# Kernel tuning notes

Hardware: AMD Instinct MI355X
Metric: run time of the kernel (lower is better)

The kernel has to match this reference:

```python
import jax, jax.numpy as jnp
import numpy as np

N_NODES = 50000
N_EDGES = 800000
IN_CH = 128
HID_CH = 128
OUT_CH = 10
NUM_GRAPHS = 128


def setup_inputs() -> dict:
    key = jax.random.key(0)
    ks = jax.random.split(key, 10)
    x = jax.random.normal(ks[0], (N_NODES, IN_CH), dtype=jnp.float32)
    edge_index = jax.random.randint(ks[1], (2, N_EDGES), 0, N_NODES, dtype=jnp.int64)
    batch = jnp.sort(jax.random.randint(ks[2], (N_NODES,), 0, NUM_GRAPHS, dtype=jnp.int64))
    s1 = 1.0 / np.sqrt(IN_CH)
    s2 = 1.0 / np.sqrt(HID_CH)
    W1 = jax.random.uniform(ks[3], (IN_CH, HID_CH), jnp.float32, -s1, s1)
    b1 = jnp.zeros((HID_CH,), jnp.float32)
    W2 = jax.random.uniform(ks[4], (HID_CH, HID_CH), jnp.float32, -s2, s2)
    b2 = jnp.zeros((HID_CH,), jnp.float32)
    Wc = jax.random.uniform(ks[5], (HID_CH, OUT_CH), jnp.float32, -s2, s2)
    bc = jax.random.uniform(ks[6], (OUT_CH,), jnp.float32, -s2, s2)
    return {"x": x, "edge_index": edge_index, "batch": batch,
            "W1": W1, "b1": b1, "W2": W2, "b2": b2, "Wc": Wc, "bc": bc}


def _gcn_norm(edge_index, num_nodes):
    # add self-loops, compute symmetric normalization deg^-1/2[src]*deg^-1/2[dst]
    loop = jnp.arange(num_nodes, dtype=edge_index.dtype)
    src = jnp.concatenate([edge_index[0], loop])
    dst = jnp.concatenate([edge_index[1], loop])
    deg = jax.ops.segment_sum(jnp.ones_like(dst, dtype=jnp.float32), dst,
                              num_segments=num_nodes)
    dinv = jnp.where(deg > 0, jax.lax.rsqrt(deg), 0.0)
    norm = dinv[src] * dinv[dst]
    return src, dst, norm


def _gcn_conv(h, src, dst, norm, W, b, num_nodes):
    h = h @ W                                    # [N, out]
    msg = h[src] * norm[:, None]                 # [E+N, out] gather + scale
    agg = jax.ops.segment_sum(msg, dst, num_segments=num_nodes)
    return agg + b


def reference(x, edge_index, batch, W1, b1, W2, b2, Wc, bc):
    n = x.shape[0]
    src, dst, norm = _gcn_norm(edge_index, n)
    h = jax.nn.relu(_gcn_conv(x, src, dst, norm, W1, b1, n))
    h = jax.nn.relu(_gcn_conv(h, src, dst, norm, W2, b2, n))
    # global mean pool over graphs
    sums = jax.ops.segment_sum(h, batch, num_segments=NUM_GRAPHS)
    cnts = jax.ops.segment_sum(jnp.ones((n,), jnp.float32), batch,
                               num_segments=NUM_GRAPHS)
    pooled = sums / jnp.maximum(cnts, 1.0)[:, None]
    # dropout is identity in eval mode
    return pooled @ Wc + bc
```

## Files before the change

### kernel.cpp

```cpp
#include <hip/hip_runtime.h>

#define N_NODES 50000
#define N_EDGES 800000
#define CH 128
#define NOUT 10
#define NUM_GRAPHS 128
#define POOL_CHUNK 50
#define GR 64
#define GEMM_BLOCKS ((N_NODES + GR - 1) / GR)
#define FILL_SEGS 128
#define FILL_CHUNK (N_EDGES / FILL_SEGS)
#define DST_RANGE (N_NODES / 8)
#define DEG_CAP 64

typedef __attribute__((ext_vector_type(8))) short bf16x8;
typedef __attribute__((ext_vector_type(4))) float f32x4;

union FragU { uint4 u; bf16x8 s; };

__device__ __forceinline__ unsigned pack_bf16(float a, float b) {
    unsigned ua = __float_as_uint(a), ub = __float_as_uint(b);
    ua += 0x7fffu + ((ua >> 16) & 1u);
    ub += 0x7fffu + ((ub >> 16) & 1u);
    return (ua >> 16) | (ub & 0xffff0000u);
}

__device__ __forceinline__ unsigned short cvt_bf16(float v) {
    unsigned u = __float_as_uint(v);
    u += 0x7fffu + ((u >> 16) & 1u);
    return (unsigned short)(u >> 16);
}

__global__ __launch_bounds__(256) void k_prep(const float* __restrict__ W1,
                                              const float* __restrict__ W2,
                                              unsigned short* __restrict__ Wb1,
                                              unsigned short* __restrict__ Wb2,
                                              int* __restrict__ fill_pos,
                                              float* __restrict__ psum) {
    if (blockIdx.x < 2) {
        const float* W = blockIdx.x ? W2 : W1;
        unsigned short* Wb = blockIdx.x ? Wb2 : Wb1;
        for (int i = threadIdx.x; i < CH * CH; i += 256) {
            int k = i >> 7, n = i & 127;
            Wb[((((k >> 3) << 7) + n) << 3) + (k & 7)] = cvt_bf16(W[i]);
        }
    } else if (blockIdx.x < 198) {
        int idx = (blockIdx.x - 2) * 256 + threadIdx.x;
        if (idx < N_NODES) fill_pos[idx] = 0;
    } else {
        psum[(blockIdx.x - 198) * 256 + threadIdx.x] = 0.f;
    }
}

template <bool SCALE>
__device__ __forceinline__ void gemm_body9(const float* __restrict__ X,
                                           const unsigned short* __restrict__ Wb,
                                           unsigned short* __restrict__ Yb,
                                           const int* __restrict__ cnt,
                                           int bid) {
    const int tid = threadIdx.x;
    const int w = tid >> 6;
    const int lane = tid & 63;
    const int m = lane & 15;
    const int quad = lane >> 4;
    const int row0 = bid * GR + w * 16;

    int row_a = row0 + m;
    if (row_a > N_NODES - 1) row_a = N_NODES - 1;
    const float4* Xr = (const float4*)(X + (size_t)row_a * CH) + quad * 2;

    f32x4 acc[8];
    #pragma unroll
    for (int ct = 0; ct < 8; ++ct) acc[ct] = (f32x4){0.f, 0.f, 0.f, 0.f};

    const uint4* Wq = (const uint4*)Wb;
    #pragma unroll
    for (int ks = 0; ks < 4; ++ks) {
        float4 a0 = Xr[ks * 8];
        float4 a1 = Xr[ks * 8 + 1];
        FragU af;
        af.u.x = pack_bf16(a0.x, a0.y);
        af.u.y = pack_bf16(a0.z, a0.w);
        af.u.z = pack_bf16(a1.x, a1.y);
        af.u.w = pack_bf16(a1.z, a1.w);
        const int kg = ks * 4 + quad;
        #pragma unroll
        for (int ct = 0; ct < 8; ++ct) {
            FragU bfu;
            bfu.u = Wq[kg * 128 + ct * 16 + m];
            acc[ct] = __builtin_amdgcn_mfma_f32_16x16x32_bf16(af.s, bfu.s, acc[ct], 0, 0, 0);
        }
    }

    #pragma unroll
    for (int r = 0; r < 4; ++r) {
        int row = row0 + quad * 4 + r;
        if (row < N_NODES) {
            float dv = SCALE ? rsqrtf((float)(cnt[row] + 1)) : 1.0f;
            unsigned short* yrow = Yb + (size_t)row * CH + m;
            #pragma unroll
            for (int ct = 0; ct < 8; ++ct)
                yrow[ct * 16] = cvt_bf16(SCALE ? acc[ct][r] * dv : acc[ct][r]);
        }
    }
}

__global__ __launch_bounds__(256) void k_gemm_fill(const float* __restrict__ X,
                                                   const unsigned short* __restrict__ Wb,
                                                   unsigned short* __restrict__ Yb,
                                                   const int* __restrict__ src,
                                                   const int* __restrict__ dst,
                                                   int* __restrict__ fill_pos,
                                                   int* __restrict__ csr_src) {
    if (blockIdx.x < GEMM_BLOCKS) {
        gemm_body9<false>(X, Wb, Yb, nullptr, blockIdx.x);
    } else {
        const int b = blockIdx.x - GEMM_BLOCKS;
        const int rng = b & 7;
        const int seg = b >> 3;
        const int lo = rng * DST_RANGE, hi = lo + DST_RANGE;
        const int base = seg * FILL_CHUNK;
        for (int it = 0; it < FILL_CHUNK; it += 256) {
            int e = base + it + threadIdx.x;
            if (it + (int)threadIdx.x < FILL_CHUNK) {
                int d = dst[e];
                if (d >= lo && d < hi) {
                    int slot = atomicAdd(&fill_pos[d], 1);
                    if (slot < DEG_CAP) csr_src[(d << 6) + slot] = src[e];
                }
            }
        }
    }
}

__global__ __launch_bounds__(256) void k_gemm9b(const float* __restrict__ X,
                                                const unsigned short* __restrict__ Wb,
                                                unsigned short* __restrict__ Yb,
                                                const int* __restrict__ cnt) {
    gemm_body9<true>(X, Wb, Yb, cnt, blockIdx.x);
}

__global__ __launch_bounds__(256) void k_gather1(const unsigned* __restrict__ tb,
                                                 const int* __restrict__ csr_src,
                                                 const int* __restrict__ cnt,
                                                 const float* __restrict__ b,
                                                 float* __restrict__ h) {
    const int wid = threadIdx.x >> 6;
    const int lane = threadIdx.x & 63;
    const int v = blockIdx.x * 4 + wid;

    int len = cnt[v];
    const float dv = rsqrtf((float)(len + 1));
    if (len > DEG_CAP) len = DEG_CAP;

    float x0 = 0.f, y0 = 0.f, x1 = 0.f, y1 = 0.f;
    float x2 = 0.f, y2 = 0.f, x3 = 0.f, y3 = 0.f;

    int u_l = 0;
    float w_l = 0.f;
    if (lane < len) {
        u_l = csr_src[(v << 6) + lane];
        w_l = rsqrtf((float)(cnt[u_l] + 1));
    }
    int j = 0;
    for (; j + 3 < len; j += 4) {
        int u0 = __shfl(u_l, j),     u1 = __shfl(u_l, j + 1);
        int u2 = __shfl(u_l, j + 2), u3 = __shfl(u_l, j + 3);
        float w0 = __shfl(w_l, j),     w1 = __shfl(w_l, j + 1);
        float w2 = __shfl(w_l, j + 2), w3 = __shfl(w_l, j + 3);
        unsigned r0 = tb[(size_t)u0 * 64 + lane];
        unsigned r1 = tb[(size_t)u1 * 64 + lane];
        unsigned r2 = tb[(size_t)u2 * 64 + lane];
        unsigned r3 = tb[(size_t)u3 * 64 + lane];
        x0 = fmaf(w0, __uint_as_float(r0 << 16), x0);
        y0 = fmaf(w0, __uint_as_float(r0 & 0xffff0000u), y0);
        x1 = fmaf(w1, __uint_as_float(r1 << 16), x1);
        y1 = fmaf(w1, __uint_as_float(r1 & 0xffff0000u), y1);
        x2 = fmaf(w2, __uint_as_float(r2 << 16), x2);
        y2 = fmaf(w2, __uint_as_float(r2 & 0xffff0000u), y2);
        x3 = fmaf(w3, __uint_as_float(r3 << 16), x3);
        y3 = fmaf(w3, __uint_as_float(r3 & 0xffff0000u), y3);
    }
    for (; j < len; ++j) {
        int u = __shfl(u_l, j);
        float w = __shfl(w_l, j);
        unsigned r = tb[(size_t)u * 64 + lane];
        x0 = fmaf(w, __uint_as_float(r << 16), x0);
        y0 = fmaf(w, __uint_as_float(r & 0xffff0000u), y0);
    }

    unsigned rs = tb[(size_t)v * 64 + lane];
    float sx = x0 + x1 + x2 + x3 + dv * __uint_as_float(rs << 16);
    float sy = y0 + y1 + y2 + y3 + dv * __uint_as_float(rs & 0xffff0000u);
    float2 bb = ((const float2*)b)[lane];
    float2 o;
    o.x = fmaxf(fmaf(dv, sx, bb.x), 0.f);
    o.y = fmaxf(fmaf(dv, sy, bb.y), 0.f);
    ((float2*)h)[(size_t)v * 64 + lane] = o;
}

__global__ __launch_bounds__(256) void k_gather2(const unsigned* __restrict__ tb,
                                                 const int* __restrict__ csr_src,
                                                 const int* __restrict__ cnt,
                                                 const float* __restrict__ b,
                                                 float* __restrict__ h) {
    const int wid = threadIdx.x >> 6;
    const int lane = threadIdx.x & 63;
    const int v = blockIdx.x * 4 + wid;

    int len = cnt[v];
    const float dv = rsqrtf((float)(len + 1));
    if (len > DEG_CAP) len = DEG_CAP;

    float x0 = 0.f, y0 = 0.f, x1 = 0.f, y1 = 0.f;
    float x2 = 0.f, y2 = 0.f, x3 = 0.f, y3 = 0.f;

    int u_l = 0;
    if (lane < len) u_l = csr_src[(v << 6) + lane];
    int j = 0;
    for (; j + 3 < len; j += 4) {
        int u0 = __shfl(u_l, j),     u1 = __shfl(u_l, j + 1);
        int u2 = __shfl(u_l, j + 2), u3 = __shfl(u_l, j + 3);
        unsigned r0 = tb[(size_t)u0 * 64 + lane];
        unsigned r1 = tb[(size_t)u1 * 64 + lane];
        unsigned r2 = tb[(size_t)u2 * 64 + lane];
        unsigned r3 = tb[(size_t)u3 * 64 + lane];
        x0 += __uint_as_float(r0 << 16); y0 += __uint_as_float(r0 & 0xffff0000u);
        x1 += __uint_as_float(r1 << 16); y1 += __uint_as_float(r1 & 0xffff0000u);
        x2 += __uint_as_float(r2 << 16); y2 += __uint_as_float(r2 & 0xffff0000u);
        x3 += __uint_as_float(r3 << 16); y3 += __uint_as_float(r3 & 0xffff0000u);
    }
    for (; j < len; ++j) {
        int u = __shfl(u_l, j);
        unsigned r = tb[(size_t)u * 64 + lane];
        x0 += __uint_as_float(r << 16); y0 += __uint_as_float(r & 0xffff0000u);
    }

    unsigned rs = tb[(size_t)v * 64 + lane];
    float sx = x0 + x1 + x2 + x3 + __uint_as_float(rs << 16);
    float sy = y0 + y1 + y2 + y3 + __uint_as_float(rs & 0xffff0000u);
    float2 bb = ((const float2*)b)[lane];
    float2 o;
    o.x = fmaxf(fmaf(dv, sx, bb.x), 0.f);
    o.y = fmaxf(fmaf(dv, sy, bb.y), 0.f);
    ((float2*)h)[(size_t)v * 64 + lane] = o;
}

__global__ __launch_bounds__(128) void k_pool2(const float* __restrict__ h,
                                               const int* __restrict__ batch,
                                               float* __restrict__ psum) {
    const int c = threadIdx.x;
    const int v0 = blockIdx.x * POOL_CHUNK;
    __shared__ int bg[POOL_CHUNK];
    if (c < POOL_CHUNK) bg[c] = batch[v0 + c];
    __syncthreads();

    float acc = 0.f;
    int g = bg[0];
    #pragma unroll 5
    for (int j = 0; j < POOL_CHUNK; ++j) {
        int bgj = bg[j];
        float val = h[(size_t)(v0 + j) * CH + c];
        if (bgj != g) {
            atomicAdd(&psum[g * CH + c], acc);
            acc = 0.f;
            g = bgj;
        }
        acc += val;
    }
    atomicAdd(&psum[g * CH + c], acc);
}

__global__ __launch_bounds__(128) void k_classify(const float* __restrict__ psum,
                                                  const int* __restrict__ batch,
                                                  const float* __restrict__ Wc,
                                                  const float* __restrict__ bc,
                                                  float* __restrict__ out) {
    __shared__ float p[CH];
    __shared__ float sinv;
    int g = blockIdx.x;
    int tid = threadIdx.x;
    if (tid == 0) {
        int lo = 0, hi = N_NODES;
        while (lo < hi) { int mid = (lo + hi) >> 1; if (batch[mid] < g) lo = mid + 1; else hi = mid; }
        int start = lo;
        lo = 0; hi = N_NODES;
        while (lo < hi) { int mid = (lo + hi) >> 1; if (batch[mid] < g + 1) lo = mid + 1; else hi = mid; }
        sinv = 1.0f / fmaxf((float)(lo - start), 1.0f);
    }
    __syncthreads();
    p[tid] = psum[g * CH + tid] * sinv;
    __syncthreads();
    if (tid < NOUT) {
        float acc = bc[tid];
        #pragma unroll 4
        for (int k = 0; k < CH; ++k) acc += p[k] * Wc[k * NOUT + tid];
        out[g * NOUT + tid] = acc;
    }
}

extern "C" void kernel_launch(void* const* d_in, const int* in_sizes, int n_in,
                              void* d_out, int out_size, void* d_ws, size_t ws_size,
                              hipStream_t stream) {
    const float* x     = (const float*)d_in[0];
    const int*   ei    = (const int*)d_in[1];
    const int*   batch = (const int*)d_in[2];
    const float* W1    = (const float*)d_in[3];
    const float* b1    = (const float*)d_in[4];
    const float* W2    = (const float*)d_in[5];
    const float* b2    = (const float*)d_in[6];
    const float* Wc    = (const float*)d_in[7];
    const float* bc    = (const float*)d_in[8];
    float* out = (float*)d_out;

    const int* src = ei;
    const int* dst = ei + N_EDGES;

    int*            fill_pos = (int*)d_ws;
    int*            csr_src  = fill_pos + N_NODES;
    unsigned short* wb1      = (unsigned short*)(csr_src + (size_t)N_NODES * DEG_CAP);
    unsigned short* wb2      = wb1 + CH * CH;
    unsigned short* tb       = wb2 + CH * CH;
    float*          hbuf     = (float*)(tb + (size_t)N_NODES * CH);
    float*          psum     = hbuf + (size_t)N_NODES * CH;

    k_prep<<<198 + 64, 256, 0, stream>>>(W1, W2, wb1, wb2, fill_pos, psum);

    k_gemm_fill<<<GEMM_BLOCKS + FILL_SEGS * 8, 256, 0, stream>>>(
        x, wb1, tb, src, dst, fill_pos, csr_src);

    k_gather1<<<N_NODES / 4, 256, 0, stream>>>((unsigned*)tb, csr_src, fill_pos, b1, hbuf);

    k_gemm9b<<<GEMM_BLOCKS, 256, 0, stream>>>(hbuf, wb2, tb, fill_pos);

    k_gather2<<<N_NODES / 4, 256, 0, stream>>>((unsigned*)tb, csr_src, fill_pos, b2, hbuf);

    k_pool2<<<N_NODES / POOL_CHUNK, 128, 0, stream>>>(hbuf, batch, psum);
    k_classify<<<NUM_GRAPHS, 128, 0, stream>>>(psum, batch, Wc, bc, out);
}
```

Baseline: 260.1 us.

## Fuse mean-pool into second gather, widen gather loads, vectorize CSR fill

The second GCN aggregation now accumulates pooled graph sums directly through shared memory and atomics, so the separate pool kernel and the store and reload of the layer-2 hidden buffer are gone. Both gather kernels switch to 16-byte loads, with each wave processing four neighbours at once in 16-lane subgroups and combining them with cross-lane shuffle reductions. The CSR fill reads dst as int4 and uses more segments, and the GEMM issues all of its X loads before the MFMA loop. In exchange it adds a block-level sync and shuffle-reduction overhead, and the fill assumes the chunk size is divisible by four.

```diff
diff --git a/kernel.cpp b/kernel.cpp
--- a/kernel.cpp
+++ b/kernel.cpp
@@ -5,10 +5,9 @@
 #define CH 128
 #define NOUT 10
 #define NUM_GRAPHS 128
-#define POOL_CHUNK 50
 #define GR 64
 #define GEMM_BLOCKS ((N_NODES + GR - 1) / GR)
-#define FILL_SEGS 128
+#define FILL_SEGS 200
 #define FILL_CHUNK (N_EDGES / FILL_SEGS)
 #define DST_RANGE (N_NODES / 8)
 #define DEG_CAP 64
@@ -69,6 +68,13 @@
     if (row_a > N_NODES - 1) row_a = N_NODES - 1;
     const float4* Xr = (const float4*)(X + (size_t)row_a * CH) + quad * 2;
 
+    float4 a[8];
+    #pragma unroll
+    for (int ks = 0; ks < 4; ++ks) {
+        a[ks * 2]     = Xr[ks * 8];
+        a[ks * 2 + 1] = Xr[ks * 8 + 1];
+    }
+
     f32x4 acc[8];
     #pragma unroll
     for (int ct = 0; ct < 8; ++ct) acc[ct] = (f32x4){0.f, 0.f, 0.f, 0.f};
@@ -76,13 +82,11 @@
     const uint4* Wq = (const uint4*)Wb;
     #pragma unroll
     for (int ks = 0; ks < 4; ++ks) {
-        float4 a0 = Xr[ks * 8];
-        float4 a1 = Xr[ks * 8 + 1];
         FragU af;
-        af.u.x = pack_bf16(a0.x, a0.y);
-        af.u.y = pack_bf16(a0.z, a0.w);
-        af.u.z = pack_bf16(a1.x, a1.y);
-        af.u.w = pack_bf16(a1.z, a1.w);
+        af.u.x = pack_bf16(a[ks * 2].x, a[ks * 2].y);
+        af.u.y = pack_bf16(a[ks * 2].z, a[ks * 2].w);
+        af.u.z = pack_bf16(a[ks * 2 + 1].x, a[ks * 2 + 1].y);
+        af.u.w = pack_bf16(a[ks * 2 + 1].z, a[ks * 2 + 1].w);
         const int kg = ks * 4 + quad;
         #pragma unroll
         for (int ct = 0; ct < 8; ++ct) {
@@ -120,13 +124,15 @@
         const int seg = b >> 3;
         const int lo = rng * DST_RANGE, hi = lo + DST_RANGE;
         const int base = seg * FILL_CHUNK;
-        for (int it = 0; it < FILL_CHUNK; it += 256) {
-            int e = base + it + threadIdx.x;
-            if (it + (int)threadIdx.x < FILL_CHUNK) {
-                int d = dst[e];
+        for (int it = threadIdx.x * 4; it < FILL_CHUNK; it += 1024) {
+            int e = base + it;
+            int4 d4 = *(const int4*)(dst + e);
+            #pragma unroll
+            for (int k = 0; k < 4; ++k) {
+                int d = (&d4.x)[k];
                 if (d >= lo && d < hi) {
                     int slot = atomicAdd(&fill_pos[d], 1);
-                    if (slot < DEG_CAP) csr_src[(d << 6) + slot] = src[e];
+                    if (slot < DEG_CAP) csr_src[(d << 6) + slot] = src[e + k];
                 }
             }
         }
@@ -140,135 +146,149 @@
     gemm_body9<true>(X, Wb, Yb, cnt, blockIdx.x);
 }
 
-__global__ __launch_bounds__(256) void k_gather1(const unsigned* __restrict__ tb,
-                                                 const int* __restrict__ csr_src,
-                                                 const int* __restrict__ cnt,
-                                                 const float* __restrict__ b,
-                                                 float* __restrict__ h) {
+template <bool HAS_W, bool POOL>
+__device__ __forceinline__ void gather_body(const unsigned* __restrict__ tb,
+                                            const int* __restrict__ csr_src,
+                                            const int* __restrict__ cnt,
+                                            const float* __restrict__ bias,
+                                            float* __restrict__ h,
+                                            const int* __restrict__ batch,
+                                            float* __restrict__ psum) {
     const int wid = threadIdx.x >> 6;
     const int lane = threadIdx.x & 63;
+    const int sub = lane >> 4;
+    const int cidx = lane & 15;
     const int v = blockIdx.x * 4 + wid;
 
-    int len = cnt[v];
-    const float dv = rsqrtf((float)(len + 1));
-    if (len > DEG_CAP) len = DEG_CAP;
-
-    float x0 = 0.f, y0 = 0.f, x1 = 0.f, y1 = 0.f;
-    float x2 = 0.f, y2 = 0.f, x3 = 0.f, y3 = 0.f;
+    int lenc = cnt[v];
+    const float dv = rsqrtf((float)(lenc + 1));
+    int len = lenc > DEG_CAP ? DEG_CAP : lenc;
 
     int u_l = 0;
     float w_l = 0.f;
     if (lane < len) {
         u_l = csr_src[(v << 6) + lane];
-        w_l = rsqrtf((float)(cnt[u_l] + 1));
-    }
+        if (HAS_W) w_l = rsqrtf((float)(cnt[u_l] + 1));
+    }
+
+    const uint4* tbq = (const uint4*)tb;
+    float x[8];
+    #pragma unroll
+    for (int t = 0; t < 8; ++t) x[t] = 0.f;
+
     int j = 0;
-    for (; j + 3 < len; j += 4) {
-        int u0 = __shfl(u_l, j),     u1 = __shfl(u_l, j + 1);
-        int u2 = __shfl(u_l, j + 2), u3 = __shfl(u_l, j + 3);
-        float w0 = __shfl(w_l, j),     w1 = __shfl(w_l, j + 1);
-        float w2 = __shfl(w_l, j + 2), w3 = __shfl(w_l, j + 3);
-        unsigned r0 = tb[(size_t)u0 * 64 + lane];
-        unsigned r1 = tb[(size_t)u1 * 64 + lane];
-        unsigned r2 = tb[(size_t)u2 * 64 + lane];
-        unsigned r3 = tb[(size_t)u3 * 64 + lane];
-        x0 = fmaf(w0, __uint_as_float(r0 << 16), x0);
-        y0 = fmaf(w0, __uint_as_float(r0 & 0xffff0000u), y0);
-        x1 = fmaf(w1, __uint_as_float(r1 << 16), x1);
-        y1 = fmaf(w1, __uint_as_float(r1 & 0xffff0000u), y1);
-        x2 = fmaf(w2, __uint_as_float(r2 << 16), x2);
-        y2 = fmaf(w2, __uint_as_float(r2 & 0xffff0000u), y2);
-        x3 = fmaf(w3, __uint_as_float(r3 << 16), x3);
-        y3 = fmaf(w3, __uint_as_float(r3 & 0xffff0000u), y3);
-    }
-    for (; j < len; ++j) {
-        int u = __shfl(u_l, j);
-        float w = __shfl(w_l, j);
-        unsigned r = tb[(size_t)u * 64 + lane];
-        x0 = fmaf(w, __uint_as_float(r << 16), x0);
-        y0 = fmaf(w, __uint_as_float(r & 0xffff0000u), y0);
-    }
-
-    unsigned rs = tb[(size_t)v * 64 + lane];
-    float sx = x0 + x1 + x2 + x3 + dv * __uint_as_float(rs << 16);
-    float sy = y0 + y1 + y2 + y3 + dv * __uint_as_float(rs & 0xffff0000u);
-    float2 bb = ((const float2*)b)[lane];
-    float2 o;
-    o.x = fmaxf(fmaf(dv, sx, bb.x), 0.f);
-    o.y = fmaxf(fmaf(dv, sy, bb.y), 0.f);
-    ((float2*)h)[(size_t)v * 64 + lane] = o;
-}
-
-__global__ __launch_bounds__(256) void k_gather2(const unsigned* __restrict__ tb,
-                                                 const int* __restrict__ csr_src,
-                                                 const int* __restrict__ cnt,
-                                                 const float* __restrict__ b,
-                                                 float* __restrict__ h) {
-    const int wid = threadIdx.x >> 6;
-    const int lane = threadIdx.x & 63;
-    const int v = blockIdx.x * 4 + wid;
-
-    int len = cnt[v];
-    const float dv = rsqrtf((float)(len + 1));
-    if (len > DEG_CAP) len = DEG_CAP;
-
-    float x0 = 0.f, y0 = 0.f, x1 = 0.f, y1 = 0.f;
-    float x2 = 0.f, y2 = 0.f, x3 = 0.f, y3 = 0.f;
-
-    int u_l = 0;
-    if (lane < len) u_l = csr_src[(v << 6) + lane];
-    int j = 0;
-    for (; j + 3 < len; j += 4) {
-        int u0 = __shfl(u_l, j),     u1 = __shfl(u_l, j + 1);
-        int u2 = __shfl(u_l, j + 2), u3 = __shfl(u_l, j + 3);
-        unsigned r0 = tb[(size_t)u0 * 64 + lane];
-        unsigned r1 = tb[(size_t)u1 * 64 + lane];
-        unsigned r2 = tb[(size_t)u2 * 64 + lane];
-        unsigned r3 = tb[(size_t)u3 * 64 + lane];
-        x0 += __uint_as_float(r0 << 16); y0 += __uint_as_float(r0 & 0xffff0000u);
-        x1 += __uint_as_float(r1 << 16); y1 += __uint_as_float(r1 & 0xffff0000u);
-        x2 += __uint_as_float(r2 << 16); y2 += __uint_as_float(r2 & 0xffff0000u);
-        x3 += __uint_as_float(r3 << 16); y3 += __uint_as_float(r3 & 0xffff0000u);
-    }
-    for (; j < len; ++j) {
-        int u = __shfl(u_l, j);
-        unsigned r = tb[(size_t)u * 64 + lane];
-        x0 += __uint_as_float(r << 16); y0 += __uint_as_float(r & 0xffff0000u);
-    }
-
-    unsigned rs = tb[(size_t)v * 64 + lane];
-    float sx = x0 + x1 + x2 + x3 + __uint_as_float(rs << 16);
-    float sy = y0 + y1 + y2 + y3 + __uint_as_float(rs & 0xffff0000u);
-    float2 bb = ((const float2*)b)[lane];
-    float2 o;
-    o.x = fmaxf(fmaf(dv, sx, bb.x), 0.f);
-    o.y = fmaxf(fmaf(dv, sy, bb.y), 0.f);
-    ((float2*)h)[(size_t)v * 64 + lane] = o;
-}
-
-__global__ __launch_bounds__(128) void k_pool2(const float* __restrict__ h,
-                                               const int* __restrict__ batch,
-                                               float* __restrict__ psum) {
-    const int c = threadIdx.x;
-    const int v0 = blockIdx.x * POOL_CHUNK;
-    __shared__ int bg[POOL_CHUNK];
-    if (c < POOL_CHUNK) bg[c] = batch[v0 + c];
-    __syncthreads();
-
-    float acc = 0.f;
-    int g = bg[0];
-    #pragma unroll 5
-    for (int j = 0; j < POOL_CHUNK; ++j) {
-        int bgj = bg[j];
-        float val = h[(size_t)(v0 + j) * CH + c];
-        if (bgj != g) {
-            atomicAdd(&psum[g * CH + c], acc);
-            acc = 0.f;
-            g = bgj;
-        }
-        acc += val;
-    }
-    atomicAdd(&psum[g * CH + c], acc);
+    for (; j + 8 <= len; j += 8) {
+        int i0 = j + sub, i1 = j + 4 + sub;
+        int ua = __shfl(u_l, i0);
+        int ub = __shfl(u_l, i1);
+        float wa = HAS_W ? __shfl(w_l, i0) : 1.f;
+        float wb = HAS_W ? __shfl(w_l, i1) : 1.f;
+        uint4 qa = tbq[(size_t)ua * 16 + cidx];
+        uint4 qb = tbq[(size_t)ub * 16 + cidx];
+        #pragma unroll
+        for (int t = 0; t < 4; ++t) {
+            unsigned ra = ((const unsigned*)&qa)[t];
+            x[2 * t]     = fmaf(wa, __uint_as_float(ra << 16), x[2 * t]);
+            x[2 * t + 1] = fmaf(wa, __uint_as_float(ra & 0xffff0000u), x[2 * t + 1]);
+        }
+        #pragma unroll
+        for (int t = 0; t < 4; ++t) {
+            unsigned rb = ((const unsigned*)&qb)[t];
+            x[2 * t]     = fmaf(wb, __uint_as_float(rb << 16), x[2 * t]);
+            x[2 * t + 1] = fmaf(wb, __uint_as_float(rb & 0xffff0000u), x[2 * t + 1]);
+        }
+    }
+    for (; j < len; j += 4) {
+        int idx = j + sub;
+        bool act = idx < len;
+        int idx_c = act ? idx : 0;
+        int u = __shfl(u_l, idx_c);
+        float w;
+        if (HAS_W) { float ws = __shfl(w_l, idx_c); w = act ? ws : 0.f; }
+        else       { w = act ? 1.f : 0.f; }
+        uint4 q = tbq[(size_t)u * 16 + cidx];
+        #pragma unroll
+        for (int t = 0; t < 4; ++t) {
+            unsigned r = ((const unsigned*)&q)[t];
+            x[2 * t]     = fmaf(w, __uint_as_float(r << 16), x[2 * t]);
+            x[2 * t + 1] = fmaf(w, __uint_as_float(r & 0xffff0000u), x[2 * t + 1]);
+        }
+    }
+    {
+        uint4 q = tbq[(size_t)v * 16 + cidx];
+        float w = (sub == 0) ? (HAS_W ? dv : 1.f) : 0.f;
+        #pragma unroll
+        for (int t = 0; t < 4; ++t) {
+            unsigned r = ((const unsigned*)&q)[t];
+            x[2 * t]     = fmaf(w, __uint_as_float(r << 16), x[2 * t]);
+            x[2 * t + 1] = fmaf(w, __uint_as_float(r & 0xffff0000u), x[2 * t + 1]);
+        }
+    }
+
+    #pragma unroll
+    for (int t = 0; t < 8; ++t) {
+        x[t] += __shfl_xor(x[t], 16);
+        x[t] += __shfl_xor(x[t], 32);
+    }
+
+    const float4* b4 = (const float4*)bias;
+    float4 b0 = b4[cidx * 2], b1 = b4[cidx * 2 + 1];
+    float4 o0, o1;
+    o0.x = fmaxf(fmaf(dv, x[0], b0.x), 0.f);
+    o0.y = fmaxf(fmaf(dv, x[1], b0.y), 0.f);
+    o0.z = fmaxf(fmaf(dv, x[2], b0.z), 0.f);
+    o0.w = fmaxf(fmaf(dv, x[3], b0.w), 0.f);
+    o1.x = fmaxf(fmaf(dv, x[4], b1.x), 0.f);
+    o1.y = fmaxf(fmaf(dv, x[5], b1.y), 0.f);
+    o1.z = fmaxf(fmaf(dv, x[6], b1.z), 0.f);
+    o1.w = fmaxf(fmaf(dv, x[7], b1.w), 0.f);
+
+    if (POOL) {
+        __shared__ float sh[4][128];
+        __shared__ int sg[4];
+        if (lane == 0) sg[wid] = batch[v];
+        if (sub == 0) {
+            *(float4*)&sh[wid][cidx * 8]     = o0;
+            *(float4*)&sh[wid][cidx * 8 + 4] = o1;
+        }
+        __syncthreads();
+        const int tid = threadIdx.x;
+        if (tid < 128) {
+            int g0 = sg[0], g1 = sg[1], g2 = sg[2], g3 = sg[3];
+            float v0 = sh[0][tid], v1 = sh[1][tid], v2 = sh[2][tid], v3 = sh[3][tid];
+            if (g0 == g3) {
+                atomicAdd(&psum[g0 * CH + tid], v0 + v1 + v2 + v3);
+            } else {
+                if (g0 == g1) v1 += v0; else atomicAdd(&psum[g0 * CH + tid], v0);
+                if (g1 == g2) v2 += v1; else atomicAdd(&psum[g1 * CH + tid], v1);
+                if (g2 == g3) v3 += v2; else atomicAdd(&psum[g2 * CH + tid], v2);
+                atomicAdd(&psum[g3 * CH + tid], v3);
+            }
+        }
+    } else {
+        if (sub == 0) {
+            float4* hq = (float4*)(h + (size_t)v * CH);
+            hq[cidx * 2]     = o0;
+            hq[cidx * 2 + 1] = o1;
+        }
+    }
+}
+
+__global__ __launch_bounds__(256) void k_gather_hw(const unsigned* __restrict__ tb,
+                                                   const int* __restrict__ csr_src,
+                                                   const int* __restrict__ cnt,
+                                                   const float* __restrict__ b,
+                                                   float* __restrict__ h) {
+    gather_body<true, false>(tb, csr_src, cnt, b, h, nullptr, nullptr);
+}
+
+__global__ __launch_bounds__(256) void k_gather_pool(const unsigned* __restrict__ tb,
+                                                     const int* __restrict__ csr_src,
+                                                     const int* __restrict__ cnt,
+                                                     const float* __restrict__ b,
+                                                     const int* __restrict__ batch,
+                                                     float* __restrict__ psum) {
+    gather_body<false, true>(tb, csr_src, cnt, b, nullptr, batch, psum);
 }
 
 __global__ __launch_bounds__(128) void k_classify(const float* __restrict__ psum,
@@ -329,12 +349,12 @@
     k_gemm_fill<<<GEMM_BLOCKS + FILL_SEGS * 8, 256, 0, stream>>>(
         x, wb1, tb, src, dst, fill_pos, csr_src);
 
-    k_gather1<<<N_NODES / 4, 256, 0, stream>>>((unsigned*)tb, csr_src, fill_pos, b1, hbuf);
+    k_gather_hw<<<N_NODES / 4, 256, 0, stream>>>((unsigned*)tb, csr_src, fill_pos, b1, hbuf);
 
     k_gemm9b<<<GEMM_BLOCKS, 256, 0, stream>>>(hbuf, wb2, tb, fill_pos);
 
-    k_gather2<<<N_NODES / 4, 256, 0, stream>>>((unsigned*)tb, csr_src, fill_pos, b2, hbuf);
-
-    k_pool2<<<N_NODES / POOL_CHUNK, 128, 0, stream>>>(hbuf, batch, psum);
+    k_gather_pool<<<N_NODES / 4, 256, 0, stream>>>((unsigned*)tb, csr_src, fill_pos, b2,
+                                                   batch, psum);
+
     k_classify<<<NUM_GRAPHS, 128, 0, stream>>>(psum, batch, Wc, bc, out);
 }
```

Result: faster. 246.5 us (-5.2%).
